# Optimization experiments

Hardware: AMD Instinct MI355X
Metric: run time of the kernel (lower is better)

Reference implementation:

```python
import jax, jax.numpy as jnp
import numpy as np

N_HEAD = 32
N_KV = 8
D = 2048
HD = D // N_HEAD
FF = 8192
EPS = 1e-5
THETA = 10000.0


def rms_norm(x, g):
    return g * x / jnp.sqrt(jnp.mean(x * x, axis=-1, keepdims=True) + EPS)


def rope(x):
    # x: [B, H, T, hd]; lucidrains interleaved RoPE
    T = x.shape[2]
    inv_freq = 1.0 / (THETA ** (jnp.arange(0, HD, 2, dtype=jnp.float32) / HD))  # [hd/2]
    freqs = jnp.arange(T, dtype=jnp.float32)[:, None] * inv_freq[None, :]       # [T, hd/2]
    freqs = jnp.repeat(freqs, 2, axis=-1)                                        # [T, hd]
    cos, sin = jnp.cos(freqs), jnp.sin(freqs)
    x1 = x[..., ::2]
    x2 = x[..., 1::2]
    rot = jnp.stack([-x2, x1], axis=-1).reshape(x.shape)
    return x * cos + rot * sin


def attention(x, wq, wk, wv, wo):
    B, T, C = x.shape
    q = (x @ wq).reshape(B, T, N_HEAD, HD).transpose(0, 2, 1, 3)  # [B,H,T,hd]
    k = (x @ wk).reshape(B, T, N_KV, HD).transpose(0, 2, 1, 3)    # [B,Hkv,T,hd]
    v = (x @ wv).reshape(B, T, N_KV, HD).transpose(0, 2, 1, 3)
    q = rope(q)
    k = rope(k)
    rep = N_HEAD // N_KV
    k = jnp.repeat(k, rep, axis=1)
    v = jnp.repeat(v, rep, axis=1)
    att = jnp.einsum('bhqd,bhkd->bhqk', q, k) * (1.0 / np.sqrt(HD))
    causal = jnp.tril(jnp.ones((T, T), dtype=bool))
    att = jnp.where(causal[None, None], att, -jnp.inf)
    att = jax.nn.softmax(att, axis=-1)
    y = jnp.einsum('bhqk,bhkd->bhqd', att, v)
    y = y.transpose(0, 2, 1, 3).reshape(B, T, C)
    return y @ wo


def mlp(x, wg, wu, wd):
    return (jax.nn.silu(x @ wg) * (x @ wu)) @ wd


def setup_inputs() -> dict:
    key = jax.random.key(0)
    ks = jax.random.split(key, 9)
    s = lambda fan_in: 1.0 / np.sqrt(fan_in)
    return {
        'x': jax.random.normal(ks[0], (1, 2048, D), dtype=jnp.float32),
        'g1': jnp.ones((D,), dtype=jnp.float32),
        'wq': jax.random.normal(ks[1], (D, D), dtype=jnp.float32) * s(D),
        'wk': jax.random.normal(ks[2], (D, N_KV * HD), dtype=jnp.float32) * s(D),
        'wv': jax.random.normal(ks[3], (D, N_KV * HD), dtype=jnp.float32) * s(D),
        'wo': jax.random.normal(ks[4], (D, D), dtype=jnp.float32) * s(D),
        'g2': jnp.ones((D,), dtype=jnp.float32),
        'wg': jax.random.normal(ks[5], (D, FF), dtype=jnp.float32) * s(D),
        'wu': jax.random.normal(ks[6], (D, FF), dtype=jnp.float32) * s(D),
        'wd': jax.random.normal(ks[7], (FF, D), dtype=jnp.float32) * s(FF),
    }


def reference(x, g1, wq, wk, wv, wo, g2, wg, wu, wd):
    residual = x
    x = rms_norm(x, g1)
    x = x + attention(x, wq, wk, wv, wo)
    x = rms_norm(x, g2)
    x = x + mlp(x, wg, wu, wd)
    x = x + residual
    return x
```

## Files before the change

kernel.cpp:

```cpp
#include <hip/hip_runtime.h>
#include <cstdint>
#include <cstddef>


typedef __attribute__((ext_vector_type(8))) short short8;
typedef __attribute__((ext_vector_type(4))) float f32x4;

typedef __attribute__((address_space(1))) const void gvoid_t;
typedef __attribute__((address_space(3))) void lvoid_t;

__device__ inline unsigned short f2b(float f) {
  unsigned int u = __float_as_uint(f);
  u += 0x7fffu + ((u >> 16) & 1u);
  return (unsigned short)(u >> 16);
}
__device__ inline float b2f(unsigned short s) {
  return __uint_as_float((unsigned int)s << 16);
}

__global__ __launch_bounds__(256) void transpose_cast(
    const float* __restrict__ W, unsigned short* __restrict__ Wt,
    int R, int ldW) {
  __shared__ unsigned short s[32 * 36];
  const int r0 = blockIdx.y * 32, c0 = blockIdx.x * 32;
  const int tr = threadIdx.x >> 3, tc = (threadIdx.x & 7) << 2;
  const float4 v = *(const float4*)(W + (size_t)(r0 + tr) * ldW + c0 + tc);
  s[tr * 36 + tc + 0] = f2b(v.x);
  s[tr * 36 + tc + 1] = f2b(v.y);
  s[tr * 36 + tc + 2] = f2b(v.z);
  s[tr * 36 + tc + 3] = f2b(v.w);
  __syncthreads();
  ushort4 o;
  o.x = s[(tc + 0) * 36 + tr];
  o.y = s[(tc + 1) * 36 + tr];
  o.z = s[(tc + 2) * 36 + tr];
  o.w = s[(tc + 3) * 36 + tr];
  *(ushort4*)(Wt + (size_t)(c0 + tr) * R + r0 + tc) = o;
}

__global__ __launch_bounds__(256) void rmsnorm(
    const float* __restrict__ X, const float* __restrict__ g,
    unsigned short* __restrict__ ob) {
  const int row = blockIdx.x;
  const float* x = X + (size_t)row * 2048;
  float ss = 0.f;
  for (int i = threadIdx.x; i < 2048; i += 256) { float v = x[i]; ss += v * v; }
  for (int off = 32; off; off >>= 1) ss += __shfl_down(ss, off, 64);
  __shared__ float red[4];
  if ((threadIdx.x & 63) == 0) red[threadIdx.x >> 6] = ss;
  __syncthreads();
  const float tot = red[0] + red[1] + red[2] + red[3];
  const float r = rsqrtf(tot * (1.f / 2048.f) + 1e-5f);
  for (int i = threadIdx.x; i < 2048; i += 256)
    ob[(size_t)row * 2048 + i] = f2b(x[i] * g[i] * r);
}

__global__ __launch_bounds__(256) void add_res(
    const unsigned short* __restrict__ h2, const float* __restrict__ x,
    float* __restrict__ out) {
  const int i = blockIdx.x * 256 + threadIdx.x;
  const ushort4 h = ((const ushort4*)h2)[i];
  const float4 xv = ((const float4*)x)[i];
  float4 o;
  o.x = xv.x + b2f(h.x); o.y = xv.y + b2f(h.y);
  o.z = xv.z + b2f(h.z); o.w = xv.w + b2f(h.w);
  ((float4*)out)[i] = o;
}

__global__ __launch_bounds__(256, 2) void gemm_bt(
    const unsigned short* __restrict__ A, const unsigned short* __restrict__ Bt,
    float* Cf, unsigned short* Cb,
    const unsigned short* add1b, const float* add2,
    int N, int Kfull, int Kchunk, int epi, int Tld,
    unsigned short* Cb2, unsigned short* Cb3) {
  __shared__ unsigned short As[128 * 64];
  __shared__ unsigned short Bs[128 * 64];
  const int tid = threadIdx.x;
  const int wave = tid >> 6, lane = tid & 63;
  const int quad = lane >> 4, l16 = lane & 15;
  const int m0 = blockIdx.y * 128, n0 = blockIdx.x * 128;
  const int wr = (wave >> 1) * 64, wc = (wave & 1) * 64;
  const int Ks = blockIdx.z * Kchunk, Ke = Ks + Kchunk;

  f32x4 acc[4][4] = {};

  for (int k0 = Ks; k0 < Ke; k0 += 64) {
#pragma unroll
    for (int p = 0; p < 4; ++p) {
      const int idx = p * 256 + tid;
      const int row = idx >> 3;
      const int kc = ((idx & 7) ^ (row & 7)) * 8;
      const unsigned short* gA = A + (size_t)(m0 + row) * Kfull + k0 + kc;
      const unsigned short* gB = Bt + (size_t)(n0 + row) * Kfull + k0 + kc;
      unsigned short* lA = As + (size_t)(p * 256 + wave * 64) * 8;
      unsigned short* lB = Bs + (size_t)(p * 256 + wave * 64) * 8;
      __builtin_amdgcn_global_load_lds((gvoid_t*)gA, (lvoid_t*)lA, 16, 0, 0);
      __builtin_amdgcn_global_load_lds((gvoid_t*)gB, (lvoid_t*)lB, 16, 0, 0);
    }
    __syncthreads();

#pragma unroll
    for (int ks = 0; ks < 2; ++ks) {
      short8 af[4], bf[4];
#pragma unroll
      for (int i = 0; i < 4; ++i) {
        const int row = wr + i * 16 + l16;
        af[i] = *(const short8*)(As + row * 64 +
                                 (((ks << 2) | quad) ^ (row & 7)) * 8);
      }
#pragma unroll
      for (int j = 0; j < 4; ++j) {
        const int row = wc + j * 16 + l16;
        bf[j] = *(const short8*)(Bs + row * 64 +
                                 (((ks << 2) | quad) ^ (row & 7)) * 8);
      }
#pragma unroll
      for (int i = 0; i < 4; ++i)
#pragma unroll
        for (int j = 0; j < 4; ++j)
          acc[i][j] = __builtin_amdgcn_mfma_f32_16x16x32_bf16(
              af[i], bf[j], acc[i][j], 0, 0, 0);
    }
    __syncthreads();
  }

  if (epi == 7 && n0 >= 2560) {
#pragma unroll
    for (int i = 0; i < 4; ++i)
#pragma unroll
      for (int j = 0; j < 4; ++j) {
        const int row = m0 + wr + i * 16 + quad * 4;
        const int col = n0 + wc + j * 16 + l16 - 2560;
        ushort4 o;
        o.x = f2b(acc[i][j][0]); o.y = f2b(acc[i][j][1]);
        o.z = f2b(acc[i][j][2]); o.w = f2b(acc[i][j][3]);
        *(ushort4*)(Cb3 + (size_t)col * Tld + row) = o;
      }
    return;
  }

#pragma unroll
  for (int i = 0; i < 4; ++i)
#pragma unroll
    for (int j = 0; j < 4; ++j) {
      const int rowb = m0 + wr + i * 16 + quad * 4;
      const int col = n0 + wc + j * 16 + l16;
      float invf = 0.f, sgn = 0.f;
      if (epi == 7) {
        const int ip = (col & 63) >> 1;
        invf = __expf(-(float)ip * 0.28782313662f);
        sgn = (col & 1) ? 1.f : -1.f;
      }
#pragma unroll
      for (int r = 0; r < 4; ++r) {
        const size_t idx = (size_t)(rowb + r) * N + col;
        const float v = acc[i][j][r];
        const float p = __shfl_xor(v, 1, 64);
        if (epi == 1) {
          Cf[idx] = v + b2f(add1b[idx]);
        } else if (epi == 3) {
          const float gt = b2f(add1b[idx]);
          Cb[idx] = f2b(gt / (1.f + __expf(-gt)) * v);
        } else if (epi == 4) {
          Cb[idx] = f2b(v);
        } else if (epi == 8) {
          atomicAdd(&Cf[idx], v);
        } else {
          float sn, cs;
          __sincosf((float)(rowb + r) * invf, &sn, &cs);
          const unsigned short o = f2b(v * cs + sgn * p * sn);
          if (col < 2048)
            Cb[(size_t)(rowb + r) * 2048 + col] = o;
          else
            Cb2[(size_t)(rowb + r) * 512 + col - 2048] = o;
        }
      }
    }
}

#define PSTR 136
__global__ __launch_bounds__(256) void flash_attn(
    const unsigned short* __restrict__ Qb, const unsigned short* __restrict__ Kb,
    const unsigned short* __restrict__ Vt, unsigned short* __restrict__ Y,
    int T) {
  __shared__ char shmem[4 * 4352];

  const int tid = threadIdx.x;
  const int wave = tid >> 6, lane = tid & 63;
  const int quad = lane >> 4, l16 = lane & 15;
  const int h = blockIdx.y;
  const int qt = gridDim.x - 1 - blockIdx.x;
  const int kvh = h >> 2;
  const int qbase = qt * 16;

  short8 aQ[2];
#pragma unroll
  for (int c = 0; c < 2; ++c)
    aQ[c] = *(const short8*)(Qb + (size_t)(qbase + l16) * 2048 + h * 64 +
                             c * 32 + quad * 8);

  float m_i[4], l_i[4];
  f32x4 Oacc[4] = {};
#pragma unroll
  for (int r = 0; r < 4; ++r) { m_i[r] = -1e30f; l_i[r] = 0.f; }

  unsigned short* Pw = (unsigned short*)(shmem + wave * 4352);
  const int nchunk = (qbase + 16 + 127) >> 7;

  for (int jt = wave; jt < nchunk; jt += 4) {
    const int k0 = jt << 7;
    f32x4 S[8];
#pragma unroll
    for (int s = 0; s < 8; ++s) {
      const size_t kr = (size_t)(k0 + s * 16 + l16) * 512 + kvh * 64;
      const short8 b0 = *(const short8*)(Kb + kr + quad * 8);
      const short8 b1 = *(const short8*)(Kb + kr + 32 + quad * 8);
      f32x4 z = {};
      z = __builtin_amdgcn_mfma_f32_16x16x32_bf16(aQ[0], b0, z, 0, 0, 0);
      z = __builtin_amdgcn_mfma_f32_16x16x32_bf16(aQ[1], b1, z, 0, 0, 0);
      S[s] = z;
    }
    float tmax[4];
#pragma unroll
    for (int r = 0; r < 4; ++r) {
      const int qrow = qbase + quad * 4 + r;
      float mx = -3e38f;
#pragma unroll
      for (int s = 0; s < 8; ++s) {
        const int key = k0 + s * 16 + l16;
        float v = S[s][r] * 0.125f;
        if (key > qrow) v = -3e38f;
        S[s][r] = v;
        mx = fmaxf(mx, v);
      }
      tmax[r] = mx;
    }
#pragma unroll
    for (int off = 1; off < 16; off <<= 1)
#pragma unroll
      for (int r = 0; r < 4; ++r)
        tmax[r] = fmaxf(tmax[r], __shfl_xor(tmax[r], off, 64));

    float alpha[4], rsum[4];
#pragma unroll
    for (int r = 0; r < 4; ++r) {
      const float mn = fmaxf(m_i[r], tmax[r]);
      alpha[r] = __expf(m_i[r] - mn);
      m_i[r] = mn;
      float acc = 0.f;
#pragma unroll
      for (int s = 0; s < 8; ++s) {
        const float p = __expf(S[s][r] - mn);
        S[s][r] = p;
        acc += p;
      }
      rsum[r] = acc;
    }
#pragma unroll
    for (int off = 1; off < 16; off <<= 1)
#pragma unroll
      for (int r = 0; r < 4; ++r)
        rsum[r] += __shfl_xor(rsum[r], off, 64);
#pragma unroll
    for (int r = 0; r < 4; ++r) l_i[r] = l_i[r] * alpha[r] + rsum[r];

#pragma unroll
    for (int s = 0; s < 8; ++s)
#pragma unroll
      for (int r = 0; r < 4; ++r)
        Pw[(quad * 4 + r) * PSTR + s * 16 + l16] = f2b(S[s][r]);
    __threadfence_block();
    short8 aP[4];
#pragma unroll
    for (int kc = 0; kc < 4; ++kc)
      aP[kc] = *(const short8*)(Pw + l16 * PSTR + kc * 32 + quad * 8);

#pragma unroll
    for (int c = 0; c < 4; ++c)
#pragma unroll
      for (int r = 0; r < 4; ++r) Oacc[c][r] *= alpha[r];
#pragma unroll
    for (int c = 0; c < 4; ++c) {
      const size_t vr = (size_t)(kvh * 64 + c * 16 + l16) * T + k0;
#pragma unroll
      for (int kc = 0; kc < 4; ++kc) {
        const short8 bV = *(const short8*)(Vt + vr + kc * 32 + quad * 8);
        Oacc[c] = __builtin_amdgcn_mfma_f32_16x16x32_bf16(aP[kc], bV,
                                                          Oacc[c], 0, 0, 0);
      }
    }
  }

  float* OWw = (float*)(shmem + wave * 4352);
  float* mw  = (float*)(shmem + wave * 4352 + 4096);
  float* lw  = (float*)(shmem + wave * 4352 + 4160);
#pragma unroll
  for (int c = 0; c < 4; ++c)
#pragma unroll
    for (int r = 0; r < 4; ++r)
      OWw[c * 256 + (quad * 4 + r) * 16 + l16] = Oacc[c][r];
  if (l16 == 0)
#pragma unroll
    for (int r = 0; r < 4; ++r) {
      mw[quad * 4 + r] = m_i[r];
      lw[quad * 4 + r] = l_i[r];
    }
  __syncthreads();

  const int c = wave;
#pragma unroll
  for (int r = 0; r < 4; ++r) {
    const int row = quad * 4 + r;
    float M = -3e38f;
#pragma unroll
    for (int w2 = 0; w2 < 4; ++w2)
      M = fmaxf(M, ((const float*)(shmem + w2 * 4352 + 4096))[row]);
    float num = 0.f, den = 0.f;
#pragma unroll
    for (int w2 = 0; w2 < 4; ++w2) {
      const float mv = ((const float*)(shmem + w2 * 4352 + 4096))[row];
      const float lv = ((const float*)(shmem + w2 * 4352 + 4160))[row];
      const float sc = __expf(mv - M);
      den += lv * sc;
      num += ((const float*)(shmem + w2 * 4352))[c * 256 + row * 16 + l16] * sc;
    }
    Y[(size_t)(qbase + row) * 2048 + h * 64 + c * 16 + l16] = f2b(num / den);
  }
}

extern "C" void kernel_launch(void* const* d_in, const int* in_sizes, int n_in,
                              void* d_out, int out_size, void* d_ws,
                              size_t ws_size, hipStream_t stream) {
  const float* x  = (const float*)d_in[0];
  const float* g1 = (const float*)d_in[1];
  const float* wq = (const float*)d_in[2];
  const float* wk = (const float*)d_in[3];
  const float* wv = (const float*)d_in[4];
  const float* wo = (const float*)d_in[5];
  const float* g2 = (const float*)d_in[6];
  const float* wg = (const float*)d_in[7];
  const float* wu = (const float*)d_in[8];
  const float* wd = (const float*)d_in[9];
  float* out = (float*)d_out;

  const int T = 2048, Dm = 2048, FF = 8192;
  char* ws = (char*)d_ws;
  const size_t MB = (size_t)1 << 20;

  unsigned short* wq_t = (unsigned short*)(ws + 0 * MB);
  unsigned short* wk_t = (unsigned short*)(ws + 8 * MB);
  unsigned short* wv_t = (unsigned short*)(ws + 10 * MB);
  unsigned short* wo_t = (unsigned short*)(ws + 12 * MB);
  unsigned short* wg_t = (unsigned short*)(ws + 20 * MB);
  unsigned short* wu_t = (unsigned short*)(ws + 52 * MB);
  unsigned short* h1_b = (unsigned short*)(ws + 84 * MB);
  unsigned short* h2_b = (unsigned short*)(ws + 92 * MB);
  float*          x2_f = (float*)(ws + 100 * MB);
  unsigned short* gate = (unsigned short*)(ws + 100 * MB);
  unsigned short* q_b  = (unsigned short*)(ws + 132 * MB);
  unsigned short* k_b  = (unsigned short*)(ws + 140 * MB);
  unsigned short* vt_b = (unsigned short*)(ws + 142 * MB);
  unsigned short* y_b  = (unsigned short*)(ws + 144 * MB);
  unsigned short* wd_t = (unsigned short*)(ws + 132 * MB);

  transpose_cast<<<dim3(64, 64), 256, 0, stream>>>(wq, wq_t, Dm, Dm);
  transpose_cast<<<dim3(16, 64), 256, 0, stream>>>(wk, wk_t, Dm, 512);
  transpose_cast<<<dim3(16, 64), 256, 0, stream>>>(wv, wv_t, Dm, 512);
  transpose_cast<<<dim3(64, 64), 256, 0, stream>>>(wo, wo_t, Dm, Dm);
  transpose_cast<<<dim3(256, 64), 256, 0, stream>>>(wg, wg_t, Dm, FF);
  transpose_cast<<<dim3(256, 64), 256, 0, stream>>>(wu, wu_t, Dm, FF);

  rmsnorm<<<T, 256, 0, stream>>>(x, g1, h1_b);

  gemm_bt<<<dim3(24, 16), 256, 0, stream>>>(h1_b, wq_t, nullptr, q_b, nullptr,
                                            nullptr, 3072, Dm, Dm, 7, T, k_b,
                                            vt_b);

  flash_attn<<<dim3(T / 16, 32), 256, 0, stream>>>(q_b, k_b, vt_b, y_b, T);

  gemm_bt<<<dim3(16, 16), 256, 0, stream>>>(y_b, wo_t, x2_f, nullptr, h1_b,
                                            nullptr, Dm, Dm, Dm, 1, 0, nullptr,
                                            nullptr);

  transpose_cast<<<dim3(64, 256), 256, 0, stream>>>(wd, wd_t, FF, Dm);

  rmsnorm<<<T, 256, 0, stream>>>(x2_f, g2, h2_b);

  gemm_bt<<<dim3(64, 16), 256, 0, stream>>>(h2_b, wg_t, nullptr, gate, nullptr,
                                            nullptr, FF, Dm, Dm, 4, 0, nullptr,
                                            nullptr);
  gemm_bt<<<dim3(64, 16), 256, 0, stream>>>(h2_b, wu_t, nullptr, gate, gate,
                                            nullptr, FF, Dm, Dm, 3, 0, nullptr,
                                            nullptr);

  add_res<<<(T * Dm / 4) / 256, 256, 0, stream>>>(h2_b, x, out);
  gemm_bt<<<dim3(16, 16, 4), 256, 0, stream>>>(gate, wd_t, out, nullptr,
                                               nullptr, nullptr, Dm, FF,
                                               FF / 4, 8, 0, nullptr, nullptr);
}
```

Before: 817.6 us.

## Transpose flash attention to compute S^T, keep P in registers

Swaps the MFMA operand order so the score tile is computed transposed (keys along rows, queries along lanes). Each lane then owns a single query, so the row max and sum need only two cross-quad shuffles, and P can feed the PV MFMA directly as the B operand through the 16x16x16 bf16 instruction, with no LDS round trip. It also folds the 1/sqrt(d) scale into Q before the loop and vectorizes the output store. The cost is extra rounding of Q to bf16 after scaling, and twice as many smaller MFMAs for PV.

```diff
diff --git a/kernel.cpp b/kernel.cpp
--- a/kernel.cpp
+++ b/kernel.cpp
@@ -4,6 +4,7 @@
 
 
 typedef __attribute__((ext_vector_type(8))) short short8;
+typedef __attribute__((ext_vector_type(4))) short s4b;
 typedef __attribute__((ext_vector_type(4))) float f32x4;
 
 typedef __attribute__((address_space(1))) const void gvoid_t;
@@ -178,12 +179,12 @@
     }
 }
 
-#define PSTR 136
+#define SLICE 4352
 __global__ __launch_bounds__(256) void flash_attn(
     const unsigned short* __restrict__ Qb, const unsigned short* __restrict__ Kb,
     const unsigned short* __restrict__ Vt, unsigned short* __restrict__ Y,
     int T) {
-  __shared__ char shmem[4 * 4352];
+  __shared__ char shmem[4 * SLICE];
 
   const int tid = threadIdx.x;
   const int wave = tid >> 6, lane = tid & 63;
@@ -192,19 +193,22 @@
   const int qt = gridDim.x - 1 - blockIdx.x;
   const int kvh = h >> 2;
   const int qbase = qt * 16;
-
-  short8 aQ[2];
-#pragma unroll
-  for (int c = 0; c < 2; ++c)
-    aQ[c] = *(const short8*)(Qb + (size_t)(qbase + l16) * 2048 + h * 64 +
-                             c * 32 + quad * 8);
-
-  float m_i[4], l_i[4];
+  const int qabs = qbase + l16;
+
+  short8 bQ[2];
+#pragma unroll
+  for (int c = 0; c < 2; ++c) {
+    short8 q = *(const short8*)(Qb + (size_t)(qbase + l16) * 2048 + h * 64 +
+                                c * 32 + quad * 8);
+#pragma unroll
+    for (int j = 0; j < 8; ++j)
+      q[j] = (short)f2b(b2f((unsigned short)q[j]) * 0.125f);
+    bQ[c] = q;
+  }
+
+  float m_i = -1e30f, l_i = 0.f;
   f32x4 Oacc[4] = {};
-#pragma unroll
-  for (int r = 0; r < 4; ++r) { m_i[r] = -1e30f; l_i[r] = 0.f; }
-
-  unsigned short* Pw = (unsigned short*)(shmem + wave * 4352);
+
   const int nchunk = (qbase + 16 + 127) >> 7;
 
   for (int jt = wave; jt < nchunk; jt += 4) {
@@ -213,119 +217,100 @@
 #pragma unroll
     for (int s = 0; s < 8; ++s) {
       const size_t kr = (size_t)(k0 + s * 16 + l16) * 512 + kvh * 64;
-      const short8 b0 = *(const short8*)(Kb + kr + quad * 8);
-      const short8 b1 = *(const short8*)(Kb + kr + 32 + quad * 8);
+      const short8 aK0 = *(const short8*)(Kb + kr + quad * 8);
+      const short8 aK1 = *(const short8*)(Kb + kr + 32 + quad * 8);
       f32x4 z = {};
-      z = __builtin_amdgcn_mfma_f32_16x16x32_bf16(aQ[0], b0, z, 0, 0, 0);
-      z = __builtin_amdgcn_mfma_f32_16x16x32_bf16(aQ[1], b1, z, 0, 0, 0);
+      z = __builtin_amdgcn_mfma_f32_16x16x32_bf16(aK0, bQ[0], z, 0, 0, 0);
+      z = __builtin_amdgcn_mfma_f32_16x16x32_bf16(aK1, bQ[1], z, 0, 0, 0);
       S[s] = z;
     }
-    float tmax[4];
-#pragma unroll
-    for (int r = 0; r < 4; ++r) {
-      const int qrow = qbase + quad * 4 + r;
-      float mx = -3e38f;
-#pragma unroll
-      for (int s = 0; s < 8; ++s) {
-        const int key = k0 + s * 16 + l16;
-        float v = S[s][r] * 0.125f;
-        if (key > qrow) v = -3e38f;
+    float mx = -3e38f;
+#pragma unroll
+    for (int s = 0; s < 8; ++s)
+#pragma unroll
+      for (int r = 0; r < 4; ++r) {
+        const int key = k0 + s * 16 + quad * 4 + r;
+        float v = S[s][r];
+        if (key > qabs) v = -3e38f;
         S[s][r] = v;
         mx = fmaxf(mx, v);
       }
-      tmax[r] = mx;
-    }
-#pragma unroll
-    for (int off = 1; off < 16; off <<= 1)
-#pragma unroll
-      for (int r = 0; r < 4; ++r)
-        tmax[r] = fmaxf(tmax[r], __shfl_xor(tmax[r], off, 64));
-
-    float alpha[4], rsum[4];
-#pragma unroll
-    for (int r = 0; r < 4; ++r) {
-      const float mn = fmaxf(m_i[r], tmax[r]);
-      alpha[r] = __expf(m_i[r] - mn);
-      m_i[r] = mn;
-      float acc = 0.f;
-#pragma unroll
-      for (int s = 0; s < 8; ++s) {
+    mx = fmaxf(mx, __shfl_xor(mx, 16, 64));
+    mx = fmaxf(mx, __shfl_xor(mx, 32, 64));
+
+    const float mn = fmaxf(m_i, mx);
+    const float alpha = __expf(m_i - mn);
+    m_i = mn;
+    float rsum = 0.f;
+    s4b bP[8];
+#pragma unroll
+    for (int s = 0; s < 8; ++s) {
+      s4b pb;
+#pragma unroll
+      for (int r = 0; r < 4; ++r) {
         const float p = __expf(S[s][r] - mn);
-        S[s][r] = p;
-        acc += p;
-      }
-      rsum[r] = acc;
-    }
-#pragma unroll
-    for (int off = 1; off < 16; off <<= 1)
-#pragma unroll
-      for (int r = 0; r < 4; ++r)
-        rsum[r] += __shfl_xor(rsum[r], off, 64);
-#pragma unroll
-    for (int r = 0; r < 4; ++r) l_i[r] = l_i[r] * alpha[r] + rsum[r];
-
-#pragma unroll
-    for (int s = 0; s < 8; ++s)
-#pragma unroll
-      for (int r = 0; r < 4; ++r)
-        Pw[(quad * 4 + r) * PSTR + s * 16 + l16] = f2b(S[s][r]);
-    __threadfence_block();
-    short8 aP[4];
-#pragma unroll
-    for (int kc = 0; kc < 4; ++kc)
-      aP[kc] = *(const short8*)(Pw + l16 * PSTR + kc * 32 + quad * 8);
+        rsum += p;
+        pb[r] = (short)f2b(p);
+      }
+      bP[s] = pb;
+    }
+    rsum += __shfl_xor(rsum, 16, 64);
+    rsum += __shfl_xor(rsum, 32, 64);
+    l_i = l_i * alpha + rsum;
 
 #pragma unroll
     for (int c = 0; c < 4; ++c)
 #pragma unroll
-      for (int r = 0; r < 4; ++r) Oacc[c][r] *= alpha[r];
+      for (int r = 0; r < 4; ++r) Oacc[c][r] *= alpha;
 #pragma unroll
     for (int c = 0; c < 4; ++c) {
       const size_t vr = (size_t)(kvh * 64 + c * 16 + l16) * T + k0;
 #pragma unroll
-      for (int kc = 0; kc < 4; ++kc) {
-        const short8 bV = *(const short8*)(Vt + vr + kc * 32 + quad * 8);
-        Oacc[c] = __builtin_amdgcn_mfma_f32_16x16x32_bf16(aP[kc], bV,
-                                                          Oacc[c], 0, 0, 0);
-      }
-    }
-  }
-
-  float* OWw = (float*)(shmem + wave * 4352);
-  float* mw  = (float*)(shmem + wave * 4352 + 4096);
-  float* lw  = (float*)(shmem + wave * 4352 + 4160);
+      for (int s = 0; s < 8; ++s) {
+        const s4b aV = *(const s4b*)(Vt + vr + s * 16 + quad * 4);
+        Oacc[c] = __builtin_amdgcn_mfma_f32_16x16x16bf16_1k(aV, bP[s],
+                                                            Oacc[c], 0, 0, 0);
+      }
+    }
+  }
+
+  float* OWw = (float*)(shmem + wave * SLICE);
+  float* mw  = (float*)(shmem + wave * SLICE + 4096);
+  float* lw  = (float*)(shmem + wave * SLICE + 4160);
 #pragma unroll
   for (int c = 0; c < 4; ++c)
 #pragma unroll
     for (int r = 0; r < 4; ++r)
       OWw[c * 256 + (quad * 4 + r) * 16 + l16] = Oacc[c][r];
-  if (l16 == 0)
-#pragma unroll
-    for (int r = 0; r < 4; ++r) {
-      mw[quad * 4 + r] = m_i[r];
-      lw[quad * 4 + r] = l_i[r];
-    }
+  if (quad == 0) { mw[l16] = m_i; lw[l16] = l_i; }
   __syncthreads();
 
   const int c = wave;
+  float M = -3e38f;
+#pragma unroll
+  for (int w2 = 0; w2 < 4; ++w2)
+    M = fmaxf(M, ((const float*)(shmem + w2 * SLICE + 4096))[l16]);
+  float den = 0.f, sc[4];
+#pragma unroll
+  for (int w2 = 0; w2 < 4; ++w2) {
+    const float mv = ((const float*)(shmem + w2 * SLICE + 4096))[l16];
+    const float lv = ((const float*)(shmem + w2 * SLICE + 4160))[l16];
+    sc[w2] = __expf(mv - M);
+    den += lv * sc[w2];
+  }
+  const float inv = 1.f / den;
+  ushort4 o;
 #pragma unroll
   for (int r = 0; r < 4; ++r) {
-    const int row = quad * 4 + r;
-    float M = -3e38f;
+    float num = 0.f;
 #pragma unroll
     for (int w2 = 0; w2 < 4; ++w2)
-      M = fmaxf(M, ((const float*)(shmem + w2 * 4352 + 4096))[row]);
-    float num = 0.f, den = 0.f;
-#pragma unroll
-    for (int w2 = 0; w2 < 4; ++w2) {
-      const float mv = ((const float*)(shmem + w2 * 4352 + 4096))[row];
-      const float lv = ((const float*)(shmem + w2 * 4352 + 4160))[row];
-      const float sc = __expf(mv - M);
-      den += lv * sc;
-      num += ((const float*)(shmem + w2 * 4352))[c * 256 + row * 16 + l16] * sc;
-    }
-    Y[(size_t)(qbase + row) * 2048 + h * 64 + c * 16 + l16] = f2b(num / den);
-  }
+      num += ((const float*)(shmem + w2 * SLICE))[c * 256 +
+                                                  (quad * 4 + r) * 16 + l16] *
+             sc[w2];
+    ((unsigned short*)&o)[r] = f2b(num * inv);
+  }
+  *(ushort4*)(Y + (size_t)(qbase + l16) * 2048 + h * 64 + c * 16 + quad * 4) = o;
 }
 
 extern "C" void kernel_launch(void* const* d_in, const int* in_sizes, int n_in,
```

Result: slower. 876.2 us (+7.2%).
